# Kernel optimization log

Hardware: AMD Instinct MI355X
Metric: run time of the kernel (lower is better)

## Reference

```python
import jax, jax.numpy as jnp
import numpy as np

H = 1024
NH = 16
HD = H // NH  # 64


def setup_inputs() -> dict:
    key = jax.random.key(0)
    ks = jax.random.split(key, 7)
    s = 1.0 / np.sqrt(H)
    return {
        "hidden_states": jax.random.normal(ks[0], (4, 2048, H), dtype=jnp.float32),
        "Wq": jax.random.normal(ks[1], (H, H), dtype=jnp.float32) * s,
        "bq": jnp.zeros((H,), dtype=jnp.float32),
        "Wk": jax.random.normal(ks[2], (H, H), dtype=jnp.float32) * s,
        "bk": jnp.zeros((H,), dtype=jnp.float32),
        "Wv": jax.random.normal(ks[3], (H, H), dtype=jnp.float32) * s,
        "bv": jnp.zeros((H,), dtype=jnp.float32),
    }


def _split_heads(x):
    # [B,S,H] -> [B,NH,S,HD]
    b, s, _ = x.shape
    return x.reshape(b, s, NH, HD).transpose(0, 2, 1, 3)


def reference(hidden_states, Wq, bq, Wk, bk, Wv, bv):
    q = _split_heads(hidden_states @ Wq + bq)
    k = _split_heads(hidden_states @ Wk + bk)
    v = _split_heads(hidden_states @ Wv + bv)
    scores = jnp.einsum("bhqd,bhkd->bhqk", q, k) / jnp.sqrt(jnp.float32(HD))
    probs = jax.nn.softmax(scores, axis=-1)  # dropout p=0 (eval) -> identity
    ctx = jnp.einsum("bhqk,bhkd->bhqd", probs, v)
    b, _, s, _ = ctx.shape
    return ctx.transpose(0, 2, 1, 3).reshape(b, s, H)
```

## Files before the change

### kernel.cpp

```cpp
#include <hip/hip_runtime.h>
#include <hip/hip_bf16.h>

#define BB  4
#define SS  2048
#define HH  1024
#define NHH 16
#define HDD 64

typedef unsigned short u16;
typedef unsigned int   u32;
using bf16x8 = __attribute__((ext_vector_type(8))) short;
using f32x4  = __attribute__((ext_vector_type(4))) float;
using f32x16 = __attribute__((ext_vector_type(16))) float;
using u32x4  = __attribute__((ext_vector_type(4))) u32;

__device__ __forceinline__ u16 f2b(float f) {
    union { float f; u32 u; } x; x.f = f;
    return (u16)((x.u + 0x7fffu + ((x.u >> 16) & 1u)) >> 16);
}
__device__ __forceinline__ u32 pk2b(float lo, float hi) {
    union { float f; u32 u; } a, b; a.f = lo; b.f = hi;
    return __builtin_amdgcn_perm(b.u + 0x8000u, a.u + 0x8000u, 0x07060302u);
}

__device__ __forceinline__ void gload16(const u16* g, u16* l) {
    __builtin_amdgcn_global_load_lds(
        (const __attribute__((address_space(1))) void*)g,
        (__attribute__((address_space(3))) void*)l, 16, 0, 0);
}

__global__ __launch_bounds__(256) void conv(
    const float* __restrict__ X,
    const float* __restrict__ Wq, const float* __restrict__ Wk,
    const float* __restrict__ Wv,
    u16* __restrict__ Xb, u16* __restrict__ Wt)
{
    const int bid = blockIdx.x;
    const int t = threadIdx.x;
    if (bid < 4096) {
        const int i = bid * 256 + t;
        float4 a = ((const float4*)X)[i * 2];
        float4 b = ((const float4*)X)[i * 2 + 1];
        ushort4 s0, s1;
        s0.x = f2b(a.x); s0.y = f2b(a.y); s0.z = f2b(a.z); s0.w = f2b(a.w);
        s1.x = f2b(b.x); s1.y = f2b(b.y); s1.z = f2b(b.z); s1.w = f2b(b.w);
        ((ushort4*)Xb)[i * 2] = s0;
        ((ushort4*)Xb)[i * 2 + 1] = s1;
        return;
    }
    const int idx = bid - 4096;
    const int z = idx >> 10, rem = idx & 1023;
    const int k0 = (rem >> 5) * 32, n0 = (rem & 31) * 32;
    const float* W = (z == 0) ? Wq : (z == 1) ? Wk : Wv;
    u16* out = Wt + (size_t)z * HH * HH;
    __shared__ float T[32][33];
    {
        const int kl = t >> 3, n4 = (t & 7) * 4;
        float4 v = *(const float4*)&W[(size_t)(k0 + kl) * HH + n0 + n4];
        T[n4 + 0][kl] = v.x; T[n4 + 1][kl] = v.y;
        T[n4 + 2][kl] = v.z; T[n4 + 3][kl] = v.w;
    }
    __syncthreads();
    {
        const int nl = t >> 3, k4 = (t & 7) * 4;
        ushort4 s;
        s.x = f2b(T[nl][k4 + 0]); s.y = f2b(T[nl][k4 + 1]);
        s.z = f2b(T[nl][k4 + 2]); s.w = f2b(T[nl][k4 + 3]);
        *(ushort4*)&out[(size_t)(n0 + nl) * HH + k0 + k4] = s;
    }
}

__global__ __launch_bounds__(256) void qkv_gemm(
    const u16* __restrict__ Xb, const u16* __restrict__ Wtb,
    const float* __restrict__ bq, const float* __restrict__ bk,
    const float* __restrict__ bv,
    u16* __restrict__ Qw, u16* __restrict__ Kw, u16* __restrict__ Vw)
{
    const int z  = blockIdx.z;
    const float* bias = (z == 0) ? bq : (z == 1) ? bk : bv;
    const int m0 = blockIdx.x * 128, n0 = blockIdx.y * 128;

    __shared__ __align__(16) u16 Xs[128 * 64];
    __shared__ __align__(16) u16 Ws[128 * 64];

    const int t = threadIdx.x;
    const int w = t >> 6, lane = t & 63, lr = lane & 15, quad = lane >> 4;
    const int l3 = lane >> 3, c7 = lane & 7;
    const int cl = (c7 ^ l3) * 8;
    const int wm = w >> 1, wn = w & 1;

    const u16* Wtz = Wtb + (size_t)z * HH * HH;

    f32x4 acc[4][4];
    #pragma unroll
    for (int i = 0; i < 4; i++)
        #pragma unroll
        for (int j = 0; j < 4; j++) acc[i][j] = f32x4{0.f, 0.f, 0.f, 0.f};

    for (int k0 = 0; k0 < HH; k0 += 64) {
        #pragma unroll
        for (int e = 0; e < 4; e++) {
            const int r = w * 32 + e * 8 + l3;
            gload16(&Xb [(size_t)(m0 + r) * HH + k0 + cl], &Xs[(w * 32 + e * 8) * 64]);
            gload16(&Wtz[(size_t)(n0 + r) * HH + k0 + cl], &Ws[(w * 32 + e * 8) * 64]);
        }
        __syncthreads();

        #pragma unroll
        for (int kc = 0; kc < 2; kc++) {
            bf16x8 af[4], bfr[4];
            const int ph = ((kc * 4 + quad) ^ c7) * 8;
            #pragma unroll
            for (int mi = 0; mi < 4; mi++)
                af[mi] = *(const bf16x8*)&Xs[(wm * 64 + mi * 16 + lr) * 64 + ph];
            #pragma unroll
            for (int ni = 0; ni < 4; ni++)
                bfr[ni] = *(const bf16x8*)&Ws[(wn * 64 + ni * 16 + lr) * 64 + ph];
            if (z != 2) {
                #pragma unroll
                for (int mi = 0; mi < 4; mi++)
                    #pragma unroll
                    for (int ni = 0; ni < 4; ni++)
                        acc[mi][ni] = __builtin_amdgcn_mfma_f32_16x16x32_bf16(
                            bfr[ni], af[mi], acc[mi][ni], 0, 0, 0);
            } else {
                #pragma unroll
                for (int mi = 0; mi < 4; mi++)
                    #pragma unroll
                    for (int ni = 0; ni < 4; ni++)
                        acc[mi][ni] = __builtin_amdgcn_mfma_f32_16x16x32_bf16(
                            af[mi], bfr[ni], acc[mi][ni], 0, 0, 0);
            }
        }
        __syncthreads();
    }

    if (z != 2) {
        u16* dst = (z == 0) ? Qw : Kw;
        const float cs = (z == 0) ? 0.18033688011112042f : 1.0f;
        #pragma unroll
        for (int mi = 0; mi < 4; mi++) {
            const int sg = m0 + wm * 64 + mi * 16 + lr;
            const int b = sg >> 11, s = sg & 2047;
            #pragma unroll
            for (int ni = 0; ni < 4; ni++) {
                const int nb = n0 + wn * 64 + ni * 16 + quad * 4;
                const int h = nb >> 6, d0 = nb & 63;
                float4 bb4 = *(const float4*)&bias[nb];
                ushort4 vs;
                vs.x = f2b((acc[mi][ni][0] + bb4.x) * cs);
                vs.y = f2b((acc[mi][ni][1] + bb4.y) * cs);
                vs.z = f2b((acc[mi][ni][2] + bb4.z) * cs);
                vs.w = f2b((acc[mi][ni][3] + bb4.w) * cs);
                *(ushort4*)&dst[((size_t)(b * NHH + h) * SS + s) * HDD + d0] = vs;
            }
        }
    } else {
        #pragma unroll
        for (int mi = 0; mi < 4; mi++)
            #pragma unroll
            for (int ni = 0; ni < 4; ni++) {
                const int mb = m0 + wm * 64 + mi * 16 + quad * 4;
                const int b = mb >> 11, s0 = mb & 2047;
                const int n = n0 + wn * 64 + ni * 16 + lr;
                const int h = n >> 6, d = n & 63;
                const float bv4 = bias[n];
                ushort4 vs;
                vs.x = f2b(acc[mi][ni][0] + bv4);
                vs.y = f2b(acc[mi][ni][1] + bv4);
                vs.z = f2b(acc[mi][ni][2] + bv4);
                vs.w = f2b(acc[mi][ni][3] + bv4);
                *(ushort4*)&Vw[((size_t)(b * NHH + h) * HDD + d) * SS + s0] = vs;
            }
    }
}

__global__ __launch_bounds__(512, 4) void attn(
    const u16* __restrict__ Qb, const u16* __restrict__ Kb,
    const u16* __restrict__ Vtb, float* __restrict__ Out)
{
    const int bid = blockIdx.x;
    const int hh = bid & 63, qt = bid >> 6;
    const int b = hh >> 4, h = hh & 15;
    const size_t hb = (size_t)hh * SS * HDD;

    __shared__ __align__(16) u16 Ks[2][64 * 64];
    __shared__ __align__(16) u16 Vs[2][64 * 64];

    const int t = threadIdx.x;
    const int w = t >> 6, lane = t & 63;
    const int q32 = lane & 31, hi = lane >> 5;
    const int l3 = lane >> 3, c7 = lane & 7;
    const int cl = (c7 ^ l3) * 8;

    bf16x8 qf[4];
    {
        const size_t qrow = (size_t)(qt * 256 + w * 32 + q32);
        #pragma unroll
        for (int ds = 0; ds < 4; ds++)
            qf[ds] = *(const bf16x8*)&Qb[hb + qrow * HDD + ds * 16 + hi * 8];
    }

    {
        const int r8 = w * 8 + l3;
        gload16(&Kb [hb + (size_t)r8 * HDD + cl], &Ks[0][w * 8 * 64]);
        gload16(&Vtb[hb + (size_t)r8 * SS + cl],  &Vs[0][w * 8 * 64]);
    }
    __syncthreads();

    float lsum = 0.f;
    f32x16 oc0 = {}, oc1 = {};

    for (int kt = 0; kt < SS / 64; kt++) {
        const int bb = kt & 1;
        if (kt + 1 < SS / 64) {
            const int r8 = w * 8 + l3;
            gload16(&Kb [hb + (size_t)((kt + 1) * 64 + r8) * HDD + cl],
                    &Ks[bb ^ 1][w * 8 * 64]);
            gload16(&Vtb[hb + (size_t)r8 * SS + (kt + 1) * 64 + cl],
                    &Vs[bb ^ 1][w * 8 * 64]);
        }

        f32x16 sc0 = {}, sc1 = {};
        __builtin_amdgcn_s_setprio(1);
        #pragma unroll
        for (int ds = 0; ds < 4; ds++) {
            const int ph = ((ds * 2 + hi) ^ c7) * 8;
            bf16x8 kf0 = *(const bf16x8*)&Ks[bb][q32 * 64 + ph];
            bf16x8 kf1 = *(const bf16x8*)&Ks[bb][(32 + q32) * 64 + ph];
            sc0 = __builtin_amdgcn_mfma_f32_32x32x16_bf16(kf0, qf[ds], sc0, 0, 0, 0);
            sc1 = __builtin_amdgcn_mfma_f32_32x32x16_bf16(kf1, qf[ds], sc1, 0, 0, 0);
        }
        __builtin_amdgcn_s_setprio(0);

        union PU { u32x4 u; bf16x8 v; } pa[4];
        #pragma unroll
        for (int kb = 0; kb < 2; kb++) {
            const f32x16 s = kb ? sc1 : sc0;
            float p[16];
            #pragma unroll
            for (int r = 0; r < 16; r++) p[r] = __builtin_amdgcn_exp2f(s[r]);
            lsum += ((((p[0] + p[1]) + (p[2] + p[3]))
                    + ((p[4] + p[5]) + (p[6] + p[7])))
                   + (((p[8] + p[9]) + (p[10] + p[11]))
                    + ((p[12] + p[13]) + (p[14] + p[15]))));
            u32 x0, x1, x2, x3, y0, y1, y2, y3;
            asm("v_cvt_pk_bf16_f32 %0, %1, %2" : "=v"(x0) : "v"(p[0]),  "v"(p[1]));
            asm("v_cvt_pk_bf16_f32 %0, %1, %2" : "=v"(x1) : "v"(p[2]),  "v"(p[3]));
            asm("v_cvt_pk_bf16_f32 %0, %1, %2" : "=v"(y0) : "v"(p[4]),  "v"(p[5]));
            asm("v_cvt_pk_bf16_f32 %0, %1, %2" : "=v"(y1) : "v"(p[6]),  "v"(p[7]));
            asm("v_cvt_pk_bf16_f32 %0, %1, %2" : "=v"(x2) : "v"(p[8]),  "v"(p[9]));
            asm("v_cvt_pk_bf16_f32 %0, %1, %2" : "=v"(x3) : "v"(p[10]), "v"(p[11]));
            asm("v_cvt_pk_bf16_f32 %0, %1, %2" : "=v"(y2) : "v"(p[12]), "v"(p[13]));
            asm("v_cvt_pk_bf16_f32 %0, %1, %2" : "=v"(y3) : "v"(p[14]), "v"(p[15]));
            asm("v_permlane32_swap_b32 %0, %1" : "+v"(x0), "+v"(y0));
            asm("v_permlane32_swap_b32 %0, %1" : "+v"(x1), "+v"(y1));
            asm("v_permlane32_swap_b32 %0, %1" : "+v"(x2), "+v"(y2));
            asm("v_permlane32_swap_b32 %0, %1" : "+v"(x3), "+v"(y3));
            pa[kb * 2 + 0].u = u32x4{x0, x1, y0, y1};
            pa[kb * 2 + 1].u = u32x4{x2, x3, y2, y3};
        }

        __builtin_amdgcn_s_setprio(1);
        #pragma unroll
        for (int ks = 0; ks < 4; ks++) {
            const int ph = ((ks * 2 + hi) ^ c7) * 8;
            bf16x8 vf0 = *(const bf16x8*)&Vs[bb][q32 * 64 + ph];
            bf16x8 vf1 = *(const bf16x8*)&Vs[bb][(32 + q32) * 64 + ph];
            oc0 = __builtin_amdgcn_mfma_f32_32x32x16_bf16(pa[ks].v, vf0, oc0, 0, 0, 0);
            oc1 = __builtin_amdgcn_mfma_f32_32x32x16_bf16(pa[ks].v, vf1, oc1, 0, 0, 0);
        }
        __builtin_amdgcn_s_setprio(0);
        __syncthreads();
    }

    lsum += __shfl_xor(lsum, 32);
    const float linv = 1.0f / lsum;

    #pragma unroll
    for (int r = 0; r < 16; r++) {
        const int cr = (r & 3) + 8 * (r >> 2) + 4 * hi;
        const float inv = __shfl(linv, cr);
        const int rq = qt * 256 + w * 32 + cr;
        float* o = &Out[((size_t)(b * SS + rq)) * HH + h * HDD + q32];
        o[0]  = oc0[r] * inv;
        o[32] = oc1[r] * inv;
    }
}

extern "C" void kernel_launch(void* const* d_in, const int* in_sizes, int n_in,
                              void* d_out, int out_size, void* d_ws, size_t ws_size,
                              hipStream_t stream) {
    const float* X  = (const float*)d_in[0];
    const float* Wq = (const float*)d_in[1];
    const float* bq = (const float*)d_in[2];
    const float* Wk = (const float*)d_in[3];
    const float* bk = (const float*)d_in[4];
    const float* Wv = (const float*)d_in[5];
    const float* bv = (const float*)d_in[6];
    float* Out = (float*)d_out;

    const size_t elems = (size_t)BB * SS * HH;
    u16* Qw = (u16*)d_ws;
    u16* Kw = Qw + elems;
    u16* Vw = Kw + elems;
    u16* Xb = (u16*)d_out;
    u16* Wt = Xb + elems;

    conv<<<dim3(4096 + 3072), 256, 0, stream>>>(X, Wq, Wk, Wv, Xb, Wt);
    qkv_gemm<<<dim3(64, 8, 3), 256, 0, stream>>>(Xb, Wt, bq, bk, bv, Qw, Kw, Vw);
    attn<<<dim3(512), 512, 0, stream>>>(Qw, Kw, Vw, Out);
}
```

Measured before the change: 238.1 us.

## Give each attention wave two query tiles to reuse K/V fragments

The attention kernel now uses 256 threads (4 waves) per block instead of 512, and each wave handles 64 query rows as two 32-row tiles. Each K and V fragment read from LDS feeds two MFMAs, halving LDS reads per unit of MFMA work and raising the compute-to-load ratio. Each thread issues twice as many global-to-LDS loads. The cost is more accumulator registers per wave and fewer waves per block to hide latency. Launch bounds change to (256, 2), and the softmax packing code moves into a helper.

```diff
diff --git a/kernel.cpp b/kernel.cpp
--- a/kernel.cpp
+++ b/kernel.cpp
@@ -17,10 +17,6 @@
 __device__ __forceinline__ u16 f2b(float f) {
     union { float f; u32 u; } x; x.f = f;
     return (u16)((x.u + 0x7fffu + ((x.u >> 16) & 1u)) >> 16);
-}
-__device__ __forceinline__ u32 pk2b(float lo, float hi) {
-    union { float f; u32 u; } a, b; a.f = lo; b.f = hi;
-    return __builtin_amdgcn_perm(b.u + 0x8000u, a.u + 0x8000u, 0x07060302u);
 }
 
 __device__ __forceinline__ void gload16(const u16* g, u16* l) {
@@ -175,7 +171,39 @@
     }
 }
 
-__global__ __launch_bounds__(512, 4) void attn(
+struct PU { union { u32x4 u; bf16x8 v; }; };
+
+__device__ __forceinline__ void packP(const f32x16& s0, const f32x16& s1,
+                                      PU pa[4], float& lsum) {
+    #pragma unroll
+    for (int kb = 0; kb < 2; kb++) {
+        const f32x16& s = kb ? s1 : s0;
+        float p[16];
+        #pragma unroll
+        for (int r = 0; r < 16; r++) p[r] = __builtin_amdgcn_exp2f(s[r]);
+        lsum += ((((p[0] + p[1]) + (p[2] + p[3]))
+                + ((p[4] + p[5]) + (p[6] + p[7])))
+               + (((p[8] + p[9]) + (p[10] + p[11]))
+                + ((p[12] + p[13]) + (p[14] + p[15]))));
+        u32 x0, x1, x2, x3, y0, y1, y2, y3;
+        asm("v_cvt_pk_bf16_f32 %0, %1, %2" : "=v"(x0) : "v"(p[0]),  "v"(p[1]));
+        asm("v_cvt_pk_bf16_f32 %0, %1, %2" : "=v"(x1) : "v"(p[2]),  "v"(p[3]));
+        asm("v_cvt_pk_bf16_f32 %0, %1, %2" : "=v"(y0) : "v"(p[4]),  "v"(p[5]));
+        asm("v_cvt_pk_bf16_f32 %0, %1, %2" : "=v"(y1) : "v"(p[6]),  "v"(p[7]));
+        asm("v_cvt_pk_bf16_f32 %0, %1, %2" : "=v"(x2) : "v"(p[8]),  "v"(p[9]));
+        asm("v_cvt_pk_bf16_f32 %0, %1, %2" : "=v"(x3) : "v"(p[10]), "v"(p[11]));
+        asm("v_cvt_pk_bf16_f32 %0, %1, %2" : "=v"(y2) : "v"(p[12]), "v"(p[13]));
+        asm("v_cvt_pk_bf16_f32 %0, %1, %2" : "=v"(y3) : "v"(p[14]), "v"(p[15]));
+        asm("v_permlane32_swap_b32 %0, %1" : "+v"(x0), "+v"(y0));
+        asm("v_permlane32_swap_b32 %0, %1" : "+v"(x1), "+v"(y1));
+        asm("v_permlane32_swap_b32 %0, %1" : "+v"(x2), "+v"(y2));
+        asm("v_permlane32_swap_b32 %0, %1" : "+v"(x3), "+v"(y3));
+        pa[kb * 2 + 0].u = u32x4{x0, x1, y0, y1};
+        pa[kb * 2 + 1].u = u32x4{x2, x3, y2, y3};
+    }
+}
+
+__global__ __launch_bounds__(256, 2) void attn(
     const u16* __restrict__ Qb, const u16* __restrict__ Kb,
     const u16* __restrict__ Vtb, float* __restrict__ Out)
 {
@@ -193,73 +221,59 @@
     const int l3 = lane >> 3, c7 = lane & 7;
     const int cl = (c7 ^ l3) * 8;
 
-    bf16x8 qf[4];
+    bf16x8 qfA[4], qfB[4];
     {
-        const size_t qrow = (size_t)(qt * 256 + w * 32 + q32);
-        #pragma unroll
-        for (int ds = 0; ds < 4; ds++)
-            qf[ds] = *(const bf16x8*)&Qb[hb + qrow * HDD + ds * 16 + hi * 8];
+        const size_t qrA = (size_t)(qt * 256 + w * 64 + q32);
+        #pragma unroll
+        for (int ds = 0; ds < 4; ds++) {
+            qfA[ds] = *(const bf16x8*)&Qb[hb + qrA * HDD + ds * 16 + hi * 8];
+            qfB[ds] = *(const bf16x8*)&Qb[hb + (qrA + 32) * HDD + ds * 16 + hi * 8];
+        }
     }
 
     {
-        const int r8 = w * 8 + l3;
-        gload16(&Kb [hb + (size_t)r8 * HDD + cl], &Ks[0][w * 8 * 64]);
-        gload16(&Vtb[hb + (size_t)r8 * SS + cl],  &Vs[0][w * 8 * 64]);
+        const int r0 = w * 16 + l3, r1 = r0 + 8;
+        gload16(&Kb [hb + (size_t)r0 * HDD + cl], &Ks[0][(w * 16) * 64]);
+        gload16(&Kb [hb + (size_t)r1 * HDD + cl], &Ks[0][(w * 16 + 8) * 64]);
+        gload16(&Vtb[hb + (size_t)r0 * SS + cl],  &Vs[0][(w * 16) * 64]);
+        gload16(&Vtb[hb + (size_t)r1 * SS + cl],  &Vs[0][(w * 16 + 8) * 64]);
     }
     __syncthreads();
 
-    float lsum = 0.f;
-    f32x16 oc0 = {}, oc1 = {};
+    float lsA = 0.f, lsB = 0.f;
+    f32x16 oA0 = {}, oA1 = {}, oB0 = {}, oB1 = {};
 
     for (int kt = 0; kt < SS / 64; kt++) {
         const int bb = kt & 1;
         if (kt + 1 < SS / 64) {
-            const int r8 = w * 8 + l3;
-            gload16(&Kb [hb + (size_t)((kt + 1) * 64 + r8) * HDD + cl],
-                    &Ks[bb ^ 1][w * 8 * 64]);
-            gload16(&Vtb[hb + (size_t)r8 * SS + (kt + 1) * 64 + cl],
-                    &Vs[bb ^ 1][w * 8 * 64]);
-        }
-
-        f32x16 sc0 = {}, sc1 = {};
+            const int r0 = w * 16 + l3, r1 = r0 + 8;
+            gload16(&Kb [hb + (size_t)((kt + 1) * 64 + r0) * HDD + cl],
+                    &Ks[bb ^ 1][(w * 16) * 64]);
+            gload16(&Kb [hb + (size_t)((kt + 1) * 64 + r1) * HDD + cl],
+                    &Ks[bb ^ 1][(w * 16 + 8) * 64]);
+            gload16(&Vtb[hb + (size_t)r0 * SS + (kt + 1) * 64 + cl],
+                    &Vs[bb ^ 1][(w * 16) * 64]);
+            gload16(&Vtb[hb + (size_t)r1 * SS + (kt + 1) * 64 + cl],
+                    &Vs[bb ^ 1][(w * 16 + 8) * 64]);
+        }
+
+        f32x16 sA0 = {}, sA1 = {}, sB0 = {}, sB1 = {};
         __builtin_amdgcn_s_setprio(1);
         #pragma unroll
         for (int ds = 0; ds < 4; ds++) {
             const int ph = ((ds * 2 + hi) ^ c7) * 8;
             bf16x8 kf0 = *(const bf16x8*)&Ks[bb][q32 * 64 + ph];
             bf16x8 kf1 = *(const bf16x8*)&Ks[bb][(32 + q32) * 64 + ph];
-            sc0 = __builtin_amdgcn_mfma_f32_32x32x16_bf16(kf0, qf[ds], sc0, 0, 0, 0);
-            sc1 = __builtin_amdgcn_mfma_f32_32x32x16_bf16(kf1, qf[ds], sc1, 0, 0, 0);
+            sA0 = __builtin_amdgcn_mfma_f32_32x32x16_bf16(kf0, qfA[ds], sA0, 0, 0, 0);
+            sA1 = __builtin_amdgcn_mfma_f32_32x32x16_bf16(kf1, qfA[ds], sA1, 0, 0, 0);
+            sB0 = __builtin_amdgcn_mfma_f32_32x32x16_bf16(kf0, qfB[ds], sB0, 0, 0, 0);
+            sB1 = __builtin_amdgcn_mfma_f32_32x32x16_bf16(kf1, qfB[ds], sB1, 0, 0, 0);
         }
         __builtin_amdgcn_s_setprio(0);
 
-        union PU { u32x4 u; bf16x8 v; } pa[4];
-        #pragma unroll
-        for (int kb = 0; kb < 2; kb++) {
-            const f32x16 s = kb ? sc1 : sc0;
-            float p[16];
-            #pragma unroll
-            for (int r = 0; r < 16; r++) p[r] = __builtin_amdgcn_exp2f(s[r]);
-            lsum += ((((p[0] + p[1]) + (p[2] + p[3]))
-                    + ((p[4] + p[5]) + (p[6] + p[7])))
-                   + (((p[8] + p[9]) + (p[10] + p[11]))
-                    + ((p[12] + p[13]) + (p[14] + p[15]))));
-            u32 x0, x1, x2, x3, y0, y1, y2, y3;
-            asm("v_cvt_pk_bf16_f32 %0, %1, %2" : "=v"(x0) : "v"(p[0]),  "v"(p[1]));
-            asm("v_cvt_pk_bf16_f32 %0, %1, %2" : "=v"(x1) : "v"(p[2]),  "v"(p[3]));
-            asm("v_cvt_pk_bf16_f32 %0, %1, %2" : "=v"(y0) : "v"(p[4]),  "v"(p[5]));
-            asm("v_cvt_pk_bf16_f32 %0, %1, %2" : "=v"(y1) : "v"(p[6]),  "v"(p[7]));
-            asm("v_cvt_pk_bf16_f32 %0, %1, %2" : "=v"(x2) : "v"(p[8]),  "v"(p[9]));
-            asm("v_cvt_pk_bf16_f32 %0, %1, %2" : "=v"(x3) : "v"(p[10]), "v"(p[11]));
-            asm("v_cvt_pk_bf16_f32 %0, %1, %2" : "=v"(y2) : "v"(p[12]), "v"(p[13]));
-            asm("v_cvt_pk_bf16_f32 %0, %1, %2" : "=v"(y3) : "v"(p[14]), "v"(p[15]));
-            asm("v_permlane32_swap_b32 %0, %1" : "+v"(x0), "+v"(y0));
-            asm("v_permlane32_swap_b32 %0, %1" : "+v"(x1), "+v"(y1));
-            asm("v_permlane32_swap_b32 %0, %1" : "+v"(x2), "+v"(y2));
-            asm("v_permlane32_swap_b32 %0, %1" : "+v"(x3), "+v"(y3));
-            pa[kb * 2 + 0].u = u32x4{x0, x1, y0, y1};
-            pa[kb * 2 + 1].u = u32x4{x2, x3, y2, y3};
-        }
+        PU paA[4], paB[4];
+        packP(sA0, sA1, paA, lsA);
+        packP(sB0, sB1, paB, lsB);
 
         __builtin_amdgcn_s_setprio(1);
         #pragma unroll
@@ -267,24 +281,31 @@
             const int ph = ((ks * 2 + hi) ^ c7) * 8;
             bf16x8 vf0 = *(const bf16x8*)&Vs[bb][q32 * 64 + ph];
             bf16x8 vf1 = *(const bf16x8*)&Vs[bb][(32 + q32) * 64 + ph];
-            oc0 = __builtin_amdgcn_mfma_f32_32x32x16_bf16(pa[ks].v, vf0, oc0, 0, 0, 0);
-            oc1 = __builtin_amdgcn_mfma_f32_32x32x16_bf16(pa[ks].v, vf1, oc1, 0, 0, 0);
+            oA0 = __builtin_amdgcn_mfma_f32_32x32x16_bf16(paA[ks].v, vf0, oA0, 0, 0, 0);
+            oA1 = __builtin_amdgcn_mfma_f32_32x32x16_bf16(paA[ks].v, vf1, oA1, 0, 0, 0);
+            oB0 = __builtin_amdgcn_mfma_f32_32x32x16_bf16(paB[ks].v, vf0, oB0, 0, 0, 0);
+            oB1 = __builtin_amdgcn_mfma_f32_32x32x16_bf16(paB[ks].v, vf1, oB1, 0, 0, 0);
         }
         __builtin_amdgcn_s_setprio(0);
         __syncthreads();
     }
 
-    lsum += __shfl_xor(lsum, 32);
-    const float linv = 1.0f / lsum;
+    lsA += __shfl_xor(lsA, 32);
+    lsB += __shfl_xor(lsB, 32);
+    const float invA = 1.0f / lsA, invB = 1.0f / lsB;
 
     #pragma unroll
     for (int r = 0; r < 16; r++) {
         const int cr = (r & 3) + 8 * (r >> 2) + 4 * hi;
-        const float inv = __shfl(linv, cr);
-        const int rq = qt * 256 + w * 32 + cr;
-        float* o = &Out[((size_t)(b * SS + rq)) * HH + h * HDD + q32];
-        o[0]  = oc0[r] * inv;
-        o[32] = oc1[r] * inv;
+        const float iA = __shfl(invA, cr);
+        const float iB = __shfl(invB, cr);
+        const int rqA = qt * 256 + w * 64 + cr;
+        float* oA = &Out[((size_t)(b * SS + rqA)) * HH + h * HDD + q32];
+        oA[0]  = oA0[r] * iA;
+        oA[32] = oA1[r] * iA;
+        float* oB = &Out[((size_t)(b * SS + rqA + 32)) * HH + h * HDD + q32];
+        oB[0]  = oB0[r] * iB;
+        oB[32] = oB1[r] * iB;
     }
 }
 
@@ -309,5 +330,5 @@
 
     conv<<<dim3(4096 + 3072), 256, 0, stream>>>(X, Wq, Wk, Wv, Xb, Wt);
     qkv_gemm<<<dim3(64, 8, 3), 256, 0, stream>>>(Xb, Wt, bq, bk, bv, Qw, Kw, Vw);
-    attn<<<dim3(512), 512, 0, stream>>>(Qw, Kw, Vw, Out);
-}
+    attn<<<dim3(512), 256, 0, stream>>>(Qw, Kw, Vw, Out);
+}
```

New measurement: 243.5 us. 2.3% more time.

## Double-buffer QKV GEMM with 128x256 tiles, 8 waves, and LDS-staged epilogue

Applied to the files above, without the earlier changes.

Reworks the QKV projection GEMM to 512-thread blocks covering 128x256 tiles with double-buffered LDS. The next K-tile's global-to-LDS loads are interleaved between four MFMA phases, using explicit waitcnt/barrier and setprio. The epilogue writes through a swizzled LDS buffer so the head-split Q/K/V stores become 16-byte coalesced row writes. This raises LDS use and register pressure, which may limit occupancy.

```diff
diff --git a/kernel.cpp b/kernel.cpp
--- a/kernel.cpp
+++ b/kernel.cpp
@@ -14,13 +14,15 @@
 using f32x16 = __attribute__((ext_vector_type(16))) float;
 using u32x4  = __attribute__((ext_vector_type(4))) u32;
 
+#define SBAR()   asm volatile("s_barrier" ::: "memory")
+#define WAITV0() asm volatile("s_waitcnt vmcnt(0)" ::: "memory")
+#define WAITV2() asm volatile("s_waitcnt vmcnt(2)" ::: "memory")
+#define LGKM0()  asm volatile("s_waitcnt lgkmcnt(0)" ::: "memory")
+#define SCHEDB() __builtin_amdgcn_sched_barrier(0)
+
 __device__ __forceinline__ u16 f2b(float f) {
     union { float f; u32 u; } x; x.f = f;
     return (u16)((x.u + 0x7fffu + ((x.u >> 16) & 1u)) >> 16);
-}
-__device__ __forceinline__ u32 pk2b(float lo, float hi) {
-    union { float f; u32 u; } a, b; a.f = lo; b.f = hi;
-    return __builtin_amdgcn_perm(b.u + 0x8000u, a.u + 0x8000u, 0x07060302u);
 }
 
 __device__ __forceinline__ void gload16(const u16* g, u16* l) {
@@ -70,7 +72,7 @@
     }
 }
 
-__global__ __launch_bounds__(256) void qkv_gemm(
+__global__ __launch_bounds__(512, 2) void qkv_gemm(
     const u16* __restrict__ Xb, const u16* __restrict__ Wtb,
     const float* __restrict__ bq, const float* __restrict__ bk,
     const float* __restrict__ bv,
@@ -78,18 +80,27 @@
 {
     const int z  = blockIdx.z;
     const float* bias = (z == 0) ? bq : (z == 1) ? bk : bv;
-    const int m0 = blockIdx.x * 128, n0 = blockIdx.y * 128;
-
-    __shared__ __align__(16) u16 Xs[128 * 64];
-    __shared__ __align__(16) u16 Ws[128 * 64];
+    const int m0 = blockIdx.x * 128, n0 = blockIdx.y * 256;
+
+    __shared__ __align__(16) u16 As[2][128 * 64];
+    __shared__ __align__(16) u16 Bs[2][256 * 64];
 
     const int t = threadIdx.x;
     const int w = t >> 6, lane = t & 63, lr = lane & 15, quad = lane >> 4;
     const int l3 = lane >> 3, c7 = lane & 7;
     const int cl = (c7 ^ l3) * 8;
-    const int wm = w >> 1, wn = w & 1;
+    const int wm = w >> 2, wn = w & 3;
 
     const u16* Wtz = Wtb + (size_t)z * HH * HH;
+
+    auto stageA = [&](int e, int kt, int nb) {
+        const int r = w * 16 + e * 8;
+        gload16(&Xb[(size_t)(m0 + r + l3) * HH + kt * 64 + cl], &As[nb][r * 64]);
+    };
+    auto stageB = [&](int e, int kt, int nb) {
+        const int r = w * 32 + e * 8;
+        gload16(&Wtz[(size_t)(n0 + r + l3) * HH + kt * 64 + cl], &Bs[nb][r * 64]);
+    };
 
     f32x4 acc[4][4];
     #pragma unroll
@@ -97,81 +108,195 @@
         #pragma unroll
         for (int j = 0; j < 4; j++) acc[i][j] = f32x4{0.f, 0.f, 0.f, 0.f};
 
-    for (int k0 = 0; k0 < HH; k0 += 64) {
-        #pragma unroll
-        for (int e = 0; e < 4; e++) {
-            const int r = w * 32 + e * 8 + l3;
-            gload16(&Xb [(size_t)(m0 + r) * HH + k0 + cl], &Xs[(w * 32 + e * 8) * 64]);
-            gload16(&Wtz[(size_t)(n0 + r) * HH + k0 + cl], &Ws[(w * 32 + e * 8) * 64]);
-        }
-        __syncthreads();
-
-        #pragma unroll
-        for (int kc = 0; kc < 2; kc++) {
-            bf16x8 af[4], bfr[4];
-            const int ph = ((kc * 4 + quad) ^ c7) * 8;
-            #pragma unroll
-            for (int mi = 0; mi < 4; mi++)
-                af[mi] = *(const bf16x8*)&Xs[(wm * 64 + mi * 16 + lr) * 64 + ph];
-            #pragma unroll
-            for (int ni = 0; ni < 4; ni++)
-                bfr[ni] = *(const bf16x8*)&Ws[(wn * 64 + ni * 16 + lr) * 64 + ph];
-            if (z != 2) {
-                #pragma unroll
-                for (int mi = 0; mi < 4; mi++)
-                    #pragma unroll
-                    for (int ni = 0; ni < 4; ni++)
-                        acc[mi][ni] = __builtin_amdgcn_mfma_f32_16x16x32_bf16(
-                            bfr[ni], af[mi], acc[mi][ni], 0, 0, 0);
-            } else {
-                #pragma unroll
-                for (int mi = 0; mi < 4; mi++)
-                    #pragma unroll
-                    for (int ni = 0; ni < 4; ni++)
-                        acc[mi][ni] = __builtin_amdgcn_mfma_f32_16x16x32_bf16(
-                            af[mi], bfr[ni], acc[mi][ni], 0, 0, 0);
-            }
-        }
-        __syncthreads();
-    }
+    stageA(0, 0, 0); stageA(1, 0, 0);
+    stageB(0, 0, 0); stageB(1, 0, 0); stageB(2, 0, 0); stageB(3, 0, 0);
+
+    bf16x8 af[4], bf[2];
+
+    for (int kt = 0; kt < 16; kt++) {
+        const int cur = kt & 1, nb = cur ^ 1;
+        const bool pf = (kt < 15);
+
+        if (pf) { stageA(0, kt + 1, nb); stageA(1, kt + 1, nb); WAITV2(); }
+        else    { WAITV0(); }
+        SBAR();
+        #pragma unroll
+        for (int mi = 0; mi < 4; mi++)
+            af[mi] = *(const bf16x8*)&As[cur][(wm * 64 + mi * 16 + lr) * 64
+                                              + (quad ^ c7) * 8];
+        #pragma unroll
+        for (int j = 0; j < 2; j++)
+            bf[j] = *(const bf16x8*)&Bs[cur][(wn * 64 + j * 16 + lr) * 64
+                                             + (quad ^ c7) * 8];
+        LGKM0(); SCHEDB();
+        __builtin_amdgcn_s_setprio(1);
+        if (z != 2) {
+            #pragma unroll
+            for (int mi = 0; mi < 4; mi++)
+                #pragma unroll
+                for (int j = 0; j < 2; j++)
+                    acc[mi][j] = __builtin_amdgcn_mfma_f32_16x16x32_bf16(
+                        bf[j], af[mi], acc[mi][j], 0, 0, 0);
+        } else {
+            #pragma unroll
+            for (int mi = 0; mi < 4; mi++)
+                #pragma unroll
+                for (int j = 0; j < 2; j++)
+                    acc[mi][j] = __builtin_amdgcn_mfma_f32_16x16x32_bf16(
+                        af[mi], bf[j], acc[mi][j], 0, 0, 0);
+        }
+        __builtin_amdgcn_s_setprio(0);
+        SBAR();
+
+        if (pf) { stageB(0, kt + 1, nb); stageB(1, kt + 1, nb); }
+        #pragma unroll
+        for (int j = 0; j < 2; j++)
+            bf[j] = *(const bf16x8*)&Bs[cur][(wn * 64 + (2 + j) * 16 + lr) * 64
+                                             + (quad ^ c7) * 8];
+        LGKM0(); SCHEDB();
+        __builtin_amdgcn_s_setprio(1);
+        if (z != 2) {
+            #pragma unroll
+            for (int mi = 0; mi < 4; mi++)
+                #pragma unroll
+                for (int j = 0; j < 2; j++)
+                    acc[mi][2 + j] = __builtin_amdgcn_mfma_f32_16x16x32_bf16(
+                        bf[j], af[mi], acc[mi][2 + j], 0, 0, 0);
+        } else {
+            #pragma unroll
+            for (int mi = 0; mi < 4; mi++)
+                #pragma unroll
+                for (int j = 0; j < 2; j++)
+                    acc[mi][2 + j] = __builtin_amdgcn_mfma_f32_16x16x32_bf16(
+                        af[mi], bf[j], acc[mi][2 + j], 0, 0, 0);
+        }
+        __builtin_amdgcn_s_setprio(0);
+        SBAR();
+
+        if (pf) stageB(2, kt + 1, nb);
+        #pragma unroll
+        for (int mi = 0; mi < 4; mi++)
+            af[mi] = *(const bf16x8*)&As[cur][(wm * 64 + mi * 16 + lr) * 64
+                                              + ((4 + quad) ^ c7) * 8];
+        #pragma unroll
+        for (int j = 0; j < 2; j++)
+            bf[j] = *(const bf16x8*)&Bs[cur][(wn * 64 + j * 16 + lr) * 64
+                                             + ((4 + quad) ^ c7) * 8];
+        LGKM0(); SCHEDB();
+        __builtin_amdgcn_s_setprio(1);
+        if (z != 2) {
+            #pragma unroll
+            for (int mi = 0; mi < 4; mi++)
+                #pragma unroll
+                for (int j = 0; j < 2; j++)
+                    acc[mi][j] = __builtin_amdgcn_mfma_f32_16x16x32_bf16(
+                        bf[j], af[mi], acc[mi][j], 0, 0, 0);
+        } else {
+            #pragma unroll
+            for (int mi = 0; mi < 4; mi++)
+                #pragma unroll
+                for (int j = 0; j < 2; j++)
+                    acc[mi][j] = __builtin_amdgcn_mfma_f32_16x16x32_bf16(
+                        af[mi], bf[j], acc[mi][j], 0, 0, 0);
+        }
+        __builtin_amdgcn_s_setprio(0);
+        SBAR();
+
+        if (pf) stageB(3, kt + 1, nb);
+        #pragma unroll
+        for (int j = 0; j < 2; j++)
+            bf[j] = *(const bf16x8*)&Bs[cur][(wn * 64 + (2 + j) * 16 + lr) * 64
+                                             + ((4 + quad) ^ c7) * 8];
+        LGKM0(); SCHEDB();
+        __builtin_amdgcn_s_setprio(1);
+        if (z != 2) {
+            #pragma unroll
+            for (int mi = 0; mi < 4; mi++)
+                #pragma unroll
+                for (int j = 0; j < 2; j++)
+                    acc[mi][2 + j] = __builtin_amdgcn_mfma_f32_16x16x32_bf16(
+                        bf[j], af[mi], acc[mi][2 + j], 0, 0, 0);
+        } else {
+            #pragma unroll
+            for (int mi = 0; mi < 4; mi++)
+                #pragma unroll
+                for (int j = 0; j < 2; j++)
+                    acc[mi][2 + j] = __builtin_amdgcn_mfma_f32_16x16x32_bf16(
+                        af[mi], bf[j], acc[mi][2 + j], 0, 0, 0);
+        }
+        __builtin_amdgcn_s_setprio(0);
+        SBAR();
+    }
+
+    u16* eb = (u16*)&Bs[0][0] + w * 4096;
 
     if (z != 2) {
-        u16* dst = (z == 0) ? Qw : Kw;
         const float cs = (z == 0) ? 0.18033688011112042f : 1.0f;
         #pragma unroll
         for (int mi = 0; mi < 4; mi++) {
-            const int sg = m0 + wm * 64 + mi * 16 + lr;
-            const int b = sg >> 11, s = sg & 2047;
+            const int rr = mi * 16 + lr;
             #pragma unroll
             for (int ni = 0; ni < 4; ni++) {
-                const int nb = n0 + wn * 64 + ni * 16 + quad * 4;
-                const int h = nb >> 6, d0 = nb & 63;
-                float4 bb4 = *(const float4*)&bias[nb];
+                const int nb2 = n0 + wn * 64 + ni * 16 + quad * 4;
+                float4 bb4 = *(const float4*)&bias[nb2];
                 ushort4 vs;
                 vs.x = f2b((acc[mi][ni][0] + bb4.x) * cs);
                 vs.y = f2b((acc[mi][ni][1] + bb4.y) * cs);
                 vs.z = f2b((acc[mi][ni][2] + bb4.z) * cs);
                 vs.w = f2b((acc[mi][ni][3] + bb4.w) * cs);
-                *(ushort4*)&dst[((size_t)(b * NHH + h) * SS + s) * HDD + d0] = vs;
+                const int cbyte = (ni * 16 + quad * 4) * 2;
+                *(ushort4*)((char*)eb + rr * 128 + (cbyte ^ ((rr & 7) << 4))) = vs;
             }
         }
     } else {
         #pragma unroll
-        for (int mi = 0; mi < 4; mi++)
+        for (int mi = 0; mi < 4; mi++) {
             #pragma unroll
             for (int ni = 0; ni < 4; ni++) {
-                const int mb = m0 + wm * 64 + mi * 16 + quad * 4;
-                const int b = mb >> 11, s0 = mb & 2047;
                 const int n = n0 + wn * 64 + ni * 16 + lr;
-                const int h = n >> 6, d = n & 63;
                 const float bv4 = bias[n];
                 ushort4 vs;
                 vs.x = f2b(acc[mi][ni][0] + bv4);
                 vs.y = f2b(acc[mi][ni][1] + bv4);
                 vs.z = f2b(acc[mi][ni][2] + bv4);
                 vs.w = f2b(acc[mi][ni][3] + bv4);
-                *(ushort4*)&Vw[((size_t)(b * NHH + h) * HDD + d) * SS + s0] = vs;
+                const int rr = ni * 16 + lr;
+                const int cbyte = (mi * 16 + quad * 4) * 2;
+                *(ushort4*)((char*)eb + rr * 128 + (cbyte ^ ((rr & 7) << 4))) = vs;
             }
+        }
+    }
+    LGKM0();
+    SCHEDB();
+
+    {
+        const int rg = lane >> 3;
+        const int cb = (lane & 7) * 16;
+        const int h = (n0 + wn * 64) >> 6;
+        if (z != 2) {
+            u16* dst = (z == 0) ? Qw : Kw;
+            #pragma unroll
+            for (int p = 0; p < 8; p++) {
+                const int r2 = p * 8 + rg;
+                bf16x8 rowv = *(const bf16x8*)
+                    ((char*)eb + r2 * 128 + (cb ^ ((r2 & 7) << 4)));
+                const int sg = m0 + wm * 64 + r2;
+                const int b = sg >> 11, s = sg & 2047;
+                *(bf16x8*)&dst[((size_t)(b * NHH + h) * SS + s) * HDD + (cb >> 1)]
+                    = rowv;
+            }
+        } else {
+            const int mb = m0 + wm * 64;
+            const int b = mb >> 11, s0 = mb & 2047;
+            #pragma unroll
+            for (int p = 0; p < 8; p++) {
+                const int r2 = p * 8 + rg;
+                bf16x8 rowv = *(const bf16x8*)
+                    ((char*)eb + r2 * 128 + (cb ^ ((r2 & 7) << 4)));
+                *(bf16x8*)&Vw[((size_t)(b * NHH + h) * HDD + r2) * SS + s0 + (cb >> 1)]
+                    = rowv;
+            }
+        }
     }
 }
 
@@ -308,6 +433,6 @@
     u16* Wt = Xb + elems;
 
     conv<<<dim3(4096 + 3072), 256, 0, stream>>>(X, Wq, Wk, Wv, Xb, Wt);
-    qkv_gemm<<<dim3(64, 8, 3), 256, 0, stream>>>(Xb, Wt, bq, bk, bv, Qw, Kw, Vw);
+    qkv_gemm<<<dim3(64, 4, 3), 512, 0, stream>>>(Xb, Wt, bq, bk, bv, Qw, Kw, Vw);
     attn<<<dim3(512), 512, 0, stream>>>(Qw, Kw, Vw, Out);
 }
```

New measurement: 281.7 us. +18.3%, slower.

## Double-buffer QKV GEMM LDS tiles and stage epilogue through LDS

Applied to the files above, without the earlier changes.

The QKV projection GEMM now double-buffers its X and W tiles in LDS, prefetching the next K-slice with async global-to-LDS loads while MFMAs run on the current one. It uses explicit vmcnt waits and raw barriers in place of __syncthreads. The epilogue writes each warp's 64x64 bf16 output into swizzled LDS, then reads it back as 16-byte rows so the global stores to Q/K/V are wide and coalesced. This doubles LDS use per block, and launch bounds now request two blocks per CU. The hand-placed waitcnt and barrier asm is fragile if the compiler reorders loads.

```diff
diff --git a/kernel.cpp b/kernel.cpp
--- a/kernel.cpp
+++ b/kernel.cpp
@@ -14,13 +14,15 @@
 using f32x16 = __attribute__((ext_vector_type(16))) float;
 using u32x4  = __attribute__((ext_vector_type(4))) u32;
 
+#define SBAR()   asm volatile("s_barrier" ::: "memory")
+#define WAITV0() asm volatile("s_waitcnt vmcnt(0)" ::: "memory")
+#define WAITV8() asm volatile("s_waitcnt vmcnt(8)" ::: "memory")
+#define LGKM0()  asm volatile("s_waitcnt lgkmcnt(0)" ::: "memory")
+#define SCHEDB() __builtin_amdgcn_sched_barrier(0)
+
 __device__ __forceinline__ u16 f2b(float f) {
     union { float f; u32 u; } x; x.f = f;
     return (u16)((x.u + 0x7fffu + ((x.u >> 16) & 1u)) >> 16);
-}
-__device__ __forceinline__ u32 pk2b(float lo, float hi) {
-    union { float f; u32 u; } a, b; a.f = lo; b.f = hi;
-    return __builtin_amdgcn_perm(b.u + 0x8000u, a.u + 0x8000u, 0x07060302u);
 }
 
 __device__ __forceinline__ void gload16(const u16* g, u16* l) {
@@ -70,7 +72,7 @@
     }
 }
 
-__global__ __launch_bounds__(256) void qkv_gemm(
+__global__ __launch_bounds__(256, 2) void qkv_gemm(
     const u16* __restrict__ Xb, const u16* __restrict__ Wtb,
     const float* __restrict__ bq, const float* __restrict__ bk,
     const float* __restrict__ bv,
@@ -80,8 +82,8 @@
     const float* bias = (z == 0) ? bq : (z == 1) ? bk : bv;
     const int m0 = blockIdx.x * 128, n0 = blockIdx.y * 128;
 
-    __shared__ __align__(16) u16 Xs[128 * 64];
-    __shared__ __align__(16) u16 Ws[128 * 64];
+    __shared__ __align__(16) u16 Xs[2][128 * 64];
+    __shared__ __align__(16) u16 Ws[2][128 * 64];
 
     const int t = threadIdx.x;
     const int w = t >> 6, lane = t & 63, lr = lane & 15, quad = lane >> 4;
@@ -97,14 +99,31 @@
         #pragma unroll
         for (int j = 0; j < 4; j++) acc[i][j] = f32x4{0.f, 0.f, 0.f, 0.f};
 
-    for (int k0 = 0; k0 < HH; k0 += 64) {
-        #pragma unroll
-        for (int e = 0; e < 4; e++) {
-            const int r = w * 32 + e * 8 + l3;
-            gload16(&Xb [(size_t)(m0 + r) * HH + k0 + cl], &Xs[(w * 32 + e * 8) * 64]);
-            gload16(&Wtz[(size_t)(n0 + r) * HH + k0 + cl], &Ws[(w * 32 + e * 8) * 64]);
-        }
-        __syncthreads();
+    #pragma unroll
+    for (int e = 0; e < 4; e++) {
+        const int r = w * 32 + e * 8 + l3;
+        gload16(&Xb [(size_t)(m0 + r) * HH + cl], &Xs[0][(w * 32 + e * 8) * 64]);
+        gload16(&Wtz[(size_t)(n0 + r) * HH + cl], &Ws[0][(w * 32 + e * 8) * 64]);
+    }
+
+    for (int kt = 0; kt < 16; kt++) {
+        const int cur = kt & 1;
+        if (kt < 15) {
+            const int k0 = (kt + 1) * 64;
+            #pragma unroll
+            for (int e = 0; e < 4; e++) {
+                const int r = w * 32 + e * 8 + l3;
+                gload16(&Xb [(size_t)(m0 + r) * HH + k0 + cl],
+                        &Xs[cur ^ 1][(w * 32 + e * 8) * 64]);
+                gload16(&Wtz[(size_t)(n0 + r) * HH + k0 + cl],
+                        &Ws[cur ^ 1][(w * 32 + e * 8) * 64]);
+            }
+            WAITV8();
+        } else {
+            WAITV0();
+        }
+        SBAR();
+        SCHEDB();
 
         #pragma unroll
         for (int kc = 0; kc < 2; kc++) {
@@ -112,10 +131,10 @@
             const int ph = ((kc * 4 + quad) ^ c7) * 8;
             #pragma unroll
             for (int mi = 0; mi < 4; mi++)
-                af[mi] = *(const bf16x8*)&Xs[(wm * 64 + mi * 16 + lr) * 64 + ph];
+                af[mi] = *(const bf16x8*)&Xs[cur][(wm * 64 + mi * 16 + lr) * 64 + ph];
             #pragma unroll
             for (int ni = 0; ni < 4; ni++)
-                bfr[ni] = *(const bf16x8*)&Ws[(wn * 64 + ni * 16 + lr) * 64 + ph];
+                bfr[ni] = *(const bf16x8*)&Ws[cur][(wn * 64 + ni * 16 + lr) * 64 + ph];
             if (z != 2) {
                 #pragma unroll
                 for (int mi = 0; mi < 4; mi++)
@@ -132,46 +151,79 @@
                             af[mi], bfr[ni], acc[mi][ni], 0, 0, 0);
             }
         }
-        __syncthreads();
-    }
+        SCHEDB();
+        SBAR();
+    }
+
+    u16* eb = (w < 2 ? &Xs[0][0] : &Ws[0][0]) + (w & 1) * 4096;
 
     if (z != 2) {
-        u16* dst = (z == 0) ? Qw : Kw;
         const float cs = (z == 0) ? 0.18033688011112042f : 1.0f;
         #pragma unroll
         for (int mi = 0; mi < 4; mi++) {
-            const int sg = m0 + wm * 64 + mi * 16 + lr;
-            const int b = sg >> 11, s = sg & 2047;
+            const int rr = mi * 16 + lr;
             #pragma unroll
             for (int ni = 0; ni < 4; ni++) {
                 const int nb = n0 + wn * 64 + ni * 16 + quad * 4;
-                const int h = nb >> 6, d0 = nb & 63;
                 float4 bb4 = *(const float4*)&bias[nb];
                 ushort4 vs;
                 vs.x = f2b((acc[mi][ni][0] + bb4.x) * cs);
                 vs.y = f2b((acc[mi][ni][1] + bb4.y) * cs);
                 vs.z = f2b((acc[mi][ni][2] + bb4.z) * cs);
                 vs.w = f2b((acc[mi][ni][3] + bb4.w) * cs);
-                *(ushort4*)&dst[((size_t)(b * NHH + h) * SS + s) * HDD + d0] = vs;
+                const int cbyte = (ni * 16 + quad * 4) * 2;
+                *(ushort4*)((char*)eb + rr * 128 + (cbyte ^ ((rr & 7) << 4))) = vs;
             }
         }
     } else {
         #pragma unroll
-        for (int mi = 0; mi < 4; mi++)
+        for (int mi = 0; mi < 4; mi++) {
             #pragma unroll
             for (int ni = 0; ni < 4; ni++) {
-                const int mb = m0 + wm * 64 + mi * 16 + quad * 4;
-                const int b = mb >> 11, s0 = mb & 2047;
                 const int n = n0 + wn * 64 + ni * 16 + lr;
-                const int h = n >> 6, d = n & 63;
                 const float bv4 = bias[n];
                 ushort4 vs;
                 vs.x = f2b(acc[mi][ni][0] + bv4);
                 vs.y = f2b(acc[mi][ni][1] + bv4);
                 vs.z = f2b(acc[mi][ni][2] + bv4);
                 vs.w = f2b(acc[mi][ni][3] + bv4);
-                *(ushort4*)&Vw[((size_t)(b * NHH + h) * HDD + d) * SS + s0] = vs;
-            }
+                const int rr = ni * 16 + lr;
+                const int cbyte = (mi * 16 + quad * 4) * 2;
+                *(ushort4*)((char*)eb + rr * 128 + (cbyte ^ ((rr & 7) << 4))) = vs;
+            }
+        }
+    }
+    LGKM0();
+    SCHEDB();
+
+    {
+        const int rg = lane >> 3;
+        const int cb = (lane & 7) * 16;
+        const int h = (n0 + wn * 64) >> 6;
+        if (z != 2) {
+            u16* dst = (z == 0) ? Qw : Kw;
+            #pragma unroll
+            for (int p = 0; p < 8; p++) {
+                const int r2 = p * 8 + rg;
+                bf16x8 rowv = *(const bf16x8*)
+                    ((char*)eb + r2 * 128 + (cb ^ ((r2 & 7) << 4)));
+                const int sg = m0 + wm * 64 + r2;
+                const int b = sg >> 11, s = sg & 2047;
+                *(bf16x8*)&dst[((size_t)(b * NHH + h) * SS + s) * HDD + (cb >> 1)]
+                    = rowv;
+            }
+        } else {
+            const int mb = m0 + wm * 64;
+            const int b = mb >> 11, s0 = mb & 2047;
+            #pragma unroll
+            for (int p = 0; p < 8; p++) {
+                const int r2 = p * 8 + rg;
+                bf16x8 rowv = *(const bf16x8*)
+                    ((char*)eb + r2 * 128 + (cb ^ ((r2 & 7) << 4)));
+                *(bf16x8*)&Vw[((size_t)(b * NHH + h) * HDD + r2) * SS + s0 + (cb >> 1)]
+                    = rowv;
+            }
+        }
     }
 }
 
```

New measurement: 239.6 us. About the same (+0.6%).
